# Kernel tuning notes

Measured on AMD Instinct MI355X. Metric: run time of the kernel, lower is better.

The kernel has to match this reference:

```python
import jax, jax.numpy as jnp
import numpy as np
from functools import partial

V, CTX, D, H, L, FF = 50257, 1024, 768, 12, 12, 3072
DH = D // H
EPS = 1e-5


def _ln(x, g, b):
    m = jnp.mean(x, axis=-1, keepdims=True)
    v = jnp.mean(jnp.square(x - m), axis=-1, keepdims=True)
    return (x - m) * jax.lax.rsqrt(v + EPS) * g + b


def setup_inputs() -> dict:
    key = jax.random.key(0)
    ks = jax.random.split(key, 8)
    s = 0.02
    return {
        "input_ids": jax.random.randint(ks[0], (2, 1024), 0, V),
        "token_emb": jax.random.normal(ks[1], (V, D), jnp.float32) * s,
        "pos_emb": jax.random.normal(ks[2], (CTX, D), jnp.float32) * s,
        "ln1_g": jnp.ones((L, D), jnp.float32),
        "ln1_b": jnp.zeros((L, D), jnp.float32),
        "qkv_w": jax.random.normal(ks[3], (L, 3 * D, D), jnp.float32) * s,
        "out_w": jax.random.normal(ks[4], (L, D, D), jnp.float32) * (s / np.sqrt(2 * L)),
        "ln2_g": jnp.ones((L, D), jnp.float32),
        "ln2_b": jnp.zeros((L, D), jnp.float32),
        "ff1_w": jax.random.normal(ks[5], (L, FF, D), jnp.float32) * s,
        "ff2_w": jax.random.normal(ks[6], (L, D, FF), jnp.float32) * s,
        "lnf_g": jnp.ones((D,), jnp.float32),
        "lnf_b": jnp.zeros((D,), jnp.float32),
    }


def reference(input_ids, token_emb, pos_emb, ln1_g, ln1_b, qkv_w, out_w,
              ln2_g, ln2_b, ff1_w, ff2_w, lnf_g, lnf_b):
    B, T = input_ids.shape
    x = token_emb[input_ids] + pos_emb[:T]  # [B,T,D]
    causal = jnp.tril(jnp.ones((T, T), bool))  # True = keep
    scale = 1.0 / np.sqrt(DH)

    def block(x, p):
        g1, b1, wqkv, wo, g2, b2, w1, w2 = p
        h = _ln(x, g1, b1)
        qkv = h @ wqkv.T  # [B,T,3D]
        q, k, v = jnp.split(qkv, 3, axis=-1)
        q = q.reshape(B, T, H, DH).transpose(0, 2, 1, 3)
        k = k.reshape(B, T, H, DH).transpose(0, 2, 1, 3)
        v = v.reshape(B, T, H, DH).transpose(0, 2, 1, 3)
        scores = jnp.einsum('bhqd,bhkd->bhqk', q, k) * scale
        scores = jnp.where(causal, scores, -jnp.inf)
        w = jax.nn.softmax(scores, axis=-1)
        o = jnp.einsum('bhqk,bhkd->bhqd', w, v)
        o = o.transpose(0, 2, 1, 3).reshape(B, T, D) @ wo.T
        x = x + o
        h2 = _ln(x, g2, b2)
        ff = jax.nn.gelu(h2 @ w1.T, approximate=False) @ w2.T
        return x + ff, None

    params = (ln1_g, ln1_b, qkv_w, out_w, ln2_g, ln2_b, ff1_w, ff2_w)
    x, _ = jax.lax.scan(block, x, params)
    x = _ln(x, lnf_g, lnf_b)
    logits = x @ token_emb.T  # tied lm head
    return logits
```

## Files before the change

### kernel.cpp

```cpp
#include <hip/hip_runtime.h>
#include <hip/hip_bf16.h>
#include <math.h>

#define D_MODEL 768
#define NHEAD 12
#define DHEAD 64
#define NLAYER 12
#define FF_DIM 3072
#define SEQ 1024
#define TOKENS 2048
#define VOCAB 50257

typedef short bf16x8 __attribute__((ext_vector_type(8)));
typedef float f32x4 __attribute__((ext_vector_type(4)));
typedef unsigned short u16x4 __attribute__((ext_vector_type(4)));
typedef unsigned short u16x8 __attribute__((ext_vector_type(8)));

__device__ inline unsigned short f2bf(float f) {
    union { float f; unsigned u; } un;
    un.f = f;
    unsigned u = un.u;
    u += 0x7fffu + ((u >> 16) & 1u);
    return (unsigned short)(u >> 16);
}

__device__ inline void gl_lds16(const void* g, void* l) {
    __builtin_amdgcn_global_load_lds(
        (const __attribute__((address_space(1))) unsigned int*)g,
        (__attribute__((address_space(3))) unsigned int*)l, 16, 0, 0);
}

__global__ __launch_bounds__(256) void cvt_kernel(const float* __restrict__ s,
                                                  unsigned short* __restrict__ d,
                                                  long n4) {
    long i = (long)blockIdx.x * 256 + threadIdx.x;
    long stride = (long)gridDim.x * 256;
    for (; i < n4; i += stride) {
        f32x4 v = ((const f32x4*)s)[i];
        u16x4 r;
        r[0] = f2bf(v[0]); r[1] = f2bf(v[1]); r[2] = f2bf(v[2]); r[3] = f2bf(v[3]);
        ((u16x4*)d)[i] = r;
    }
}

__global__ __launch_bounds__(256) void embed_kernel(const int* __restrict__ ids,
                                                    const float* __restrict__ tok,
                                                    const float* __restrict__ pos,
                                                    float* __restrict__ x) {
    int i = blockIdx.x * 256 + threadIdx.x;
    int row = i / D_MODEL;
    int d = i - row * D_MODEL;
    int t = row & (SEQ - 1);
    x[i] = tok[(long)ids[row] * D_MODEL + d] + pos[(long)t * D_MODEL + d];
}

__global__ __launch_bounds__(256) void ln_kernel(const float* __restrict__ x,
                                                 const float* __restrict__ g,
                                                 const float* __restrict__ b,
                                                 unsigned short* __restrict__ out) {
    int row = blockIdx.x;
    int tid = threadIdx.x;
    const float* xr = x + (long)row * D_MODEL;
    float v0 = xr[tid], v1 = xr[tid + 256], v2 = xr[tid + 512];
    __shared__ float sm[4];
    float s = v0 + v1 + v2;
    #pragma unroll
    for (int off = 32; off; off >>= 1) s += __shfl_xor(s, off);
    if ((tid & 63) == 0) sm[tid >> 6] = s;
    __syncthreads();
    float mean = (sm[0] + sm[1] + sm[2] + sm[3]) * (1.f / D_MODEL);
    __syncthreads();
    float d0 = v0 - mean, d1 = v1 - mean, d2 = v2 - mean;
    s = d0 * d0 + d1 * d1 + d2 * d2;
    #pragma unroll
    for (int off = 32; off; off >>= 1) s += __shfl_xor(s, off);
    if ((tid & 63) == 0) sm[tid >> 6] = s;
    __syncthreads();
    float var = (sm[0] + sm[1] + sm[2] + sm[3]) * (1.f / D_MODEL);
    float rs = rsqrtf(var + 1e-5f);
    unsigned short* orow = out + (long)row * D_MODEL;
    orow[tid]       = f2bf(d0 * rs * g[tid]       + b[tid]);
    orow[tid + 256] = f2bf(d1 * rs * g[tid + 256] + b[tid + 256]);
    orow[tid + 512] = f2bf(d2 * rs * g[tid + 512] + b[tid + 512]);
}

#define GM_NONE 0
#define GM_RES  1
#define GM_GELU 2
#define GM_QKV  3

template<int WM, int WN, int MODE, int DB>
__global__ __launch_bounds__(256) void gemm_bf16(
        const unsigned short* __restrict__ A, const unsigned short* __restrict__ W,
        int M, int N, int K,
        float* __restrict__ Cf, unsigned short* __restrict__ Cb,
        const float* __restrict__ RES,
        unsigned short* __restrict__ P1, unsigned short* __restrict__ P2) {
    constexpr int BM = WM * 32, BN = WN * 32;
    __shared__ unsigned short lA[DB][BM * 64];
    __shared__ unsigned short lB[DB][BN * 64];

    int tid = threadIdx.x;
    int lane = tid & 63, wv = tid >> 6;
    int wr = wv >> 1, wc = wv & 1;
    int lr = lane & 15, kq = lane >> 4;
    int row0 = blockIdx.x * BM;
    int col0 = blockIdx.y * BN;

    int srow_in = tid >> 3;
    int ssp = tid & 7;
    int skg = ssp ^ (srow_in & 7);
    int lbase = ((tid & ~63)) << 3;

    f32x4 acc[WM][WN];
    #pragma unroll
    for (int m = 0; m < WM; m++)
        #pragma unroll
        for (int n = 0; n < WN; n++) acc[m][n] = (f32x4){0.f, 0.f, 0.f, 0.f};

    auto stage = [&](int buf, int kt) {
        #pragma unroll
        for (int i = 0; i < BM / 32; i++) {
            int row = i * 32 + srow_in;
            gl_lds16(A + (size_t)(row0 + row) * K + kt + skg * 8,
                     &lA[buf][i * 2048 + lbase]);
        }
        #pragma unroll
        for (int i = 0; i < BN / 32; i++) {
            int row = i * 32 + srow_in;
            int srow = col0 + row;
            if (srow >= N) srow = N - 1;
            gl_lds16(W + (size_t)srow * K + kt + skg * 8,
                     &lB[buf][i * 2048 + lbase]);
        }
    };
    auto compute = [&](int buf) {
        #pragma unroll
        for (int kk = 0; kk < 2; kk++) {
            int kg = kk * 4 + kq;
            bf16x8 af[WM], bfr[WN];
            #pragma unroll
            for (int m = 0; m < WM; m++) {
                int row = wr * (WM * 16) + m * 16 + lr;
                af[m] = *(const bf16x8*)&lA[buf][row * 64 + ((kg ^ (row & 7)) << 3)];
            }
            #pragma unroll
            for (int n = 0; n < WN; n++) {
                int row = wc * (WN * 16) + n * 16 + lr;
                bfr[n] = *(const bf16x8*)&lB[buf][row * 64 + ((kg ^ (row & 7)) << 3)];
            }
            #pragma unroll
            for (int m = 0; m < WM; m++)
                #pragma unroll
                for (int n = 0; n < WN; n++)
                    acc[m][n] = __builtin_amdgcn_mfma_f32_16x16x32_bf16(af[m], bfr[n], acc[m][n], 0, 0, 0);
        }
    };

    if (DB == 2) {
        stage(0, 0);
        __syncthreads();
        int nt = K >> 6;
        int cur = 0;
        for (int t = 0; t < nt; t++) {
            if (t + 1 < nt) stage(cur ^ 1, (t + 1) << 6);
            compute(cur);
            __syncthreads();
            cur ^= 1;
        }
    } else {
        for (int kt = 0; kt < K; kt += 64) {
            stage(0, kt);
            __syncthreads();
            compute(0);
            __syncthreads();
        }
    }

    #pragma unroll
    for (int m = 0; m < WM; m++) {
        int r0 = row0 + wr * (WM * 16) + m * 16 + (kq << 2);
        #pragma unroll
        for (int n = 0; n < WN; n++) {
            int c = col0 + wc * (WN * 16) + n * 16 + lr;
            if (c < N) {
                #pragma unroll
                for (int j = 0; j < 4; j++) {
                    int r = r0 + j;
                    size_t idx = (size_t)r * N + c;
                    float v = acc[m][n][j];
                    if (MODE == GM_RES) {
                        Cf[idx] = v + RES[idx];
                    } else if (MODE == GM_GELU) {
                        Cb[idx] = f2bf(0.5f * v * (1.f + erff(v * 0.70710678118f)));
                    } else if (MODE == GM_QKV) {
                        int bb = r >> 10, t = r & 1023;
                        if (c < D_MODEL) {
                            int h = c >> 6, dh = c & 63;
                            P1[(((size_t)(bb * NHEAD + h) * SEQ) + t) * 64 + dh] = f2bf(v * 0.125f);
                        } else if (c < 2 * D_MODEL) {
                            int cc = c - D_MODEL;
                            int h = cc >> 6, dh = cc & 63;
                            P2[(((size_t)(bb * NHEAD + h) * SEQ) + t) * 64 + dh] = f2bf(v);
                        } else {
                            Cb[(size_t)r * D_MODEL + (c - 2 * D_MODEL)] = f2bf(v);
                        }
                    } else {
                        Cf[idx] = v;
                    }
                }
            }
        }
    }
}

__global__ __launch_bounds__(256) void vprep_kernel(const unsigned short* __restrict__ Vrow,
                                                    unsigned short* __restrict__ Vt) {
    __shared__ unsigned short T[64][66];
    int b = blockIdx.z, h = blockIdx.y, t0 = blockIdx.x * 64;
    int tid = threadIdx.x;
    int tin = tid >> 2, seg = tid & 3;
    const unsigned short* src = Vrow + ((size_t)(b * SEQ) + t0 + tin) * D_MODEL
                                + h * 64 + seg * 16;
    u16x8 a0 = *(const u16x8*)src;
    u16x8 a1 = *(const u16x8*)(src + 8);
    #pragma unroll
    for (int e = 0; e < 8; e++) { T[tin][seg * 16 + e] = a0[e]; T[tin][seg * 16 + 8 + e] = a1[e]; }
    __syncthreads();
    int dh = tid >> 2;
    unsigned short* dst = Vt + ((size_t)(b * NHEAD + h) * 64 + dh) * SEQ + t0 + seg * 16;
    u16x8 o0, o1;
    #pragma unroll
    for (int e = 0; e < 8; e++) o0[e] = T[seg * 16 + e][dh];
    #pragma unroll
    for (int e = 0; e < 8; e++) o1[e] = T[seg * 16 + 8 + e][dh];
    *(u16x8*)dst = o0;
    *(u16x8*)(dst + 8) = o1;
}

#define ANW 4
__global__ __launch_bounds__(256) void attn_mfma(const unsigned short* __restrict__ Qb,
                                                 const unsigned short* __restrict__ Kb,
                                                 const unsigned short* __restrict__ Vt,
                                                 unsigned short* __restrict__ att) {
    int b = blockIdx.z, h = blockIdx.y, pr = blockIdx.x;
    int tid = threadIdx.x, l = tid & 63, w = tid >> 6;
    int lr = l & 15, hg = l >> 4;
    int hk8 = hg * 8, hg4 = hg * 4;
    size_t bh = (size_t)b * NHEAD + h;
    const unsigned short* Qp = Qb + bh * SEQ * 64;
    const unsigned short* Kp = Kb + bh * SEQ * 64;
    const unsigned short* Vp = Vt + bh * 64 * SEQ;

    __shared__ float sm_m[ANW][2][16], sm_l[ANW][2][16];
    __shared__ float sm_o[ANW][2][16][65];
    __shared__ unsigned short pl[ANW][1024];
    unsigned short* Pw = &pl[w][0];

    #pragma unroll
    for (int ti = 0; ti < 2; ti++) {
        int tile = ti ? (63 - pr) : pr;
        int q0 = tile * 16;
        bf16x8 qf0 = *(const bf16x8*)(Qp + (size_t)(q0 + lr) * 64 + hk8);
        bf16x8 qf1 = *(const bf16x8*)(Qp + (size_t)(q0 + lr) * 64 + 32 + hk8);
        f32x4 O[4];
        #pragma unroll
        for (int dt = 0; dt < 4; dt++) O[dt] = (f32x4){0.f, 0.f, 0.f, 0.f};
        f32x4 mrun = (f32x4){-1e30f, -1e30f, -1e30f, -1e30f};
        f32x4 lrun = (f32x4){0.f, 0.f, 0.f, 0.f};
        int nch = (tile >> 2) + 1;

        for (int c = w; c < nch; c += ANW) {
            int k0 = c * 64;
            f32x4 S[4];
            #pragma unroll
            for (int kt = 0; kt < 4; kt++) {
                S[kt] = (f32x4){0.f, 0.f, 0.f, 0.f};
                bf16x8 kf = *(const bf16x8*)(Kp + (size_t)(k0 + kt * 16 + lr) * 64 + hk8);
                S[kt] = __builtin_amdgcn_mfma_f32_16x16x32_bf16(qf0, kf, S[kt], 0, 0, 0);
                kf = *(const bf16x8*)(Kp + (size_t)(k0 + kt * 16 + lr) * 64 + 32 + hk8);
                S[kt] = __builtin_amdgcn_mfma_f32_16x16x32_bf16(qf1, kf, S[kt], 0, 0, 0);
            }
            if (c == nch - 1) {
                #pragma unroll
                for (int kt = 0; kt < 4; kt++)
                    #pragma unroll
                    for (int j = 0; j < 4; j++)
                        S[kt][j] = (k0 + kt * 16 + lr <= q0 + hg4 + j) ? S[kt][j] : -3.0e38f;
            }
            f32x4 rm;
            #pragma unroll
            for (int j = 0; j < 4; j++)
                rm[j] = fmaxf(fmaxf(S[0][j], S[1][j]), fmaxf(S[2][j], S[3][j]));
            #pragma unroll
            for (int msk = 1; msk <= 8; msk <<= 1)
                #pragma unroll
                for (int j = 0; j < 4; j++)
                    rm[j] = fmaxf(rm[j], __shfl_xor(rm[j], msk));
            f32x4 mn, corr, rs;
            #pragma unroll
            for (int j = 0; j < 4; j++) {
                mn[j] = fmaxf(mrun[j], rm[j]);
                corr[j] = __expf(mrun[j] - mn[j]);
                rs[j] = 0.f;
            }
            #pragma unroll
            for (int kt = 0; kt < 4; kt++)
                #pragma unroll
                for (int j = 0; j < 4; j++) {
                    float p = __expf(S[kt][j] - mn[j]);
                    S[kt][j] = p;
                    rs[j] += p;
                }
            #pragma unroll
            for (int msk = 1; msk <= 8; msk <<= 1)
                #pragma unroll
                for (int j = 0; j < 4; j++)
                    rs[j] += __shfl_xor(rs[j], msk);
            #pragma unroll
            for (int j = 0; j < 4; j++) {
                lrun[j] = lrun[j] * corr[j] + rs[j];
                mrun[j] = mn[j];
            }
            #pragma unroll
            for (int dt = 0; dt < 4; dt++)
                #pragma unroll
                for (int j = 0; j < 4; j++) O[dt][j] *= corr[j];
            #pragma unroll
            for (int kt = 0; kt < 4; kt++) {
                int cc = kt * 16 + lr;
                int slot = cc >> 3, off = cc & 7;
                #pragma unroll
                for (int j = 0; j < 4; j++) {
                    int r = hg4 + j;
                    Pw[r * 64 + ((slot ^ (r & 7)) << 3) + off] = f2bf(S[kt][j]);
                }
            }
            asm volatile("s_waitcnt lgkmcnt(0)" ::: "memory");
            bf16x8 pf0 = *(const bf16x8*)&Pw[lr * 64 + ((hg ^ (lr & 7)) << 3)];
            bf16x8 pf1 = *(const bf16x8*)&Pw[lr * 64 + (((4 + hg) ^ (lr & 7)) << 3)];
            #pragma unroll
            for (int dt = 0; dt < 4; dt++) {
                bf16x8 vf = *(const bf16x8*)(Vp + (size_t)(dt * 16 + lr) * SEQ + k0 + hk8);
                O[dt] = __builtin_amdgcn_mfma_f32_16x16x32_bf16(pf0, vf, O[dt], 0, 0, 0);
                vf = *(const bf16x8*)(Vp + (size_t)(dt * 16 + lr) * SEQ + k0 + 32 + hk8);
                O[dt] = __builtin_amdgcn_mfma_f32_16x16x32_bf16(pf1, vf, O[dt], 0, 0, 0);
            }
        }
        if (lr == 0) {
            #pragma unroll
            for (int j = 0; j < 4; j++) {
                sm_m[w][ti][hg4 + j] = mrun[j];
                sm_l[w][ti][hg4 + j] = lrun[j];
            }
        }
        #pragma unroll
        for (int dt = 0; dt < 4; dt++)
            #pragma unroll
            for (int j = 0; j < 4; j++)
                sm_o[w][ti][hg4 + j][dt * 16 + lr] = O[dt][j];
    }
    __syncthreads();
    {
        int ti2 = w >> 1;
        int tile = ti2 ? (63 - pr) : pr;
        int q0 = tile * 16;
        #pragma unroll
        for (int jj = 0; jj < 2; jj++) {
            int j = (w & 1) * 2 + jj;
            int r = hg4 + j;
            float m0 = sm_m[0][ti2][r], m1 = sm_m[1][ti2][r];
            float m2 = sm_m[2][ti2][r], m3 = sm_m[3][ti2][r];
            float M = fmaxf(fmaxf(m0, m1), fmaxf(m2, m3));
            float e0 = __expf(m0 - M), e1 = __expf(m1 - M);
            float e2 = __expf(m2 - M), e3 = __expf(m3 - M);
            float L = sm_l[0][ti2][r] * e0 + sm_l[1][ti2][r] * e1
                    + sm_l[2][ti2][r] * e2 + sm_l[3][ti2][r] * e3;
            float invL = 1.f / L;
            unsigned short* orow = att + ((size_t)(b * SEQ + q0 + r)) * D_MODEL + h * 64;
            #pragma unroll
            for (int dt = 0; dt < 4; dt++) {
                int cidx = dt * 16 + lr;
                float o = sm_o[0][ti2][r][cidx] * e0 + sm_o[1][ti2][r][cidx] * e1
                        + sm_o[2][ti2][r][cidx] * e2 + sm_o[3][ti2][r][cidx] * e3;
                orow[cidx] = f2bf(o * invL);
            }
        }
    }
}

extern "C" void kernel_launch(void* const* d_in, const int* in_sizes, int n_in,
                              void* d_out, int out_size, void* d_ws, size_t ws_size,
                              hipStream_t stream) {
    const int*   input_ids = (const int*)d_in[0];
    const float* token_emb = (const float*)d_in[1];
    const float* pos_emb   = (const float*)d_in[2];
    const float* ln1_g     = (const float*)d_in[3];
    const float* ln1_b     = (const float*)d_in[4];
    const float* qkv_w     = (const float*)d_in[5];
    const float* out_w     = (const float*)d_in[6];
    const float* ln2_g     = (const float*)d_in[7];
    const float* ln2_b     = (const float*)d_in[8];
    const float* ff1_w     = (const float*)d_in[9];
    const float* ff2_w     = (const float*)d_in[10];
    const float* lnf_g     = (const float*)d_in[11];
    const float* lnf_b     = (const float*)d_in[12];
    float* out = (float*)d_out;

    const size_t SZ_QKV_L = (size_t)3 * D_MODEL * D_MODEL;
    const size_t SZ_OUT_L = (size_t)D_MODEL * D_MODEL;
    const size_t SZ_FF1_L = (size_t)FF_DIM * D_MODEL;
    const size_t SZ_FF2_L = (size_t)D_MODEL * FF_DIM;
    const size_t SZ_TOK   = (size_t)VOCAB * D_MODEL;

    char* base = (char*)d_ws;
    size_t off = 0;
    auto alloc = [&](size_t bytes) -> char* {
        char* p = base + off;
        off = (off + bytes + 255) & ~(size_t)255;
        return p;
    };

    float* x              = (float*)alloc((size_t)TOKENS * D_MODEL * 4);
    unsigned short* hb    = (unsigned short*)alloc((size_t)TOKENS * D_MODEL * 2);
    unsigned short* attb  = (unsigned short*)alloc((size_t)TOKENS * D_MODEL * 2);
    unsigned short* ffab  = (unsigned short*)alloc((size_t)TOKENS * FF_DIM * 2);
    unsigned short* Qb    = (unsigned short*)alloc((size_t)TOKENS * D_MODEL * 2);
    unsigned short* Kb    = (unsigned short*)alloc((size_t)TOKENS * D_MODEL * 2);
    unsigned short* Vrow  = (unsigned short*)alloc((size_t)TOKENS * D_MODEL * 2);
    unsigned short* Vtb   = (unsigned short*)alloc((size_t)TOKENS * D_MODEL * 2);

    size_t act_end = off;
    size_t full_need = act_end + 2 * (NLAYER * (SZ_QKV_L + SZ_OUT_L + SZ_FF1_L + SZ_FF2_L) + SZ_TOK)
                       + 6 * 256;
    bool full = ws_size >= full_need;

    unsigned short *qkvA, *outA, *ff1A, *ff2A, *tokA;
    if (full) {
        qkvA = (unsigned short*)alloc(2 * NLAYER * SZ_QKV_L);
        outA = (unsigned short*)alloc(2 * NLAYER * SZ_OUT_L);
        ff1A = (unsigned short*)alloc(2 * NLAYER * SZ_FF1_L);
        ff2A = (unsigned short*)alloc(2 * NLAYER * SZ_FF2_L);
        tokA = (unsigned short*)alloc(2 * SZ_TOK);
    } else {
        qkvA = (unsigned short*)alloc(2 * SZ_QKV_L);
        outA = (unsigned short*)alloc(2 * SZ_OUT_L);
        ff1A = (unsigned short*)alloc(2 * SZ_FF1_L);
        ff2A = (unsigned short*)alloc(2 * SZ_FF2_L);
        tokA = (unsigned short*)alloc(2 * SZ_TOK);
    }

    auto cvt = [&](const float* s, unsigned short* d, size_t n) {
        long n4 = (long)(n / 4);
        int g = (int)((n4 + 255) / 256);
        if (g > 2048) g = 2048;
        cvt_kernel<<<g, 256, 0, stream>>>(s, d, n4);
    };

    if (full) {
        cvt(qkv_w, qkvA, NLAYER * SZ_QKV_L);
        cvt(out_w, outA, NLAYER * SZ_OUT_L);
        cvt(ff1_w, ff1A, NLAYER * SZ_FF1_L);
        cvt(ff2_w, ff2A, NLAYER * SZ_FF2_L);
        cvt(token_emb, tokA, SZ_TOK);
    }

    embed_kernel<<<TOKENS * D_MODEL / 256, 256, 0, stream>>>(input_ids, token_emb, pos_emb, x);

    for (int l = 0; l < NLAYER; l++) {
        const unsigned short* qw = full ? qkvA + (size_t)l * SZ_QKV_L : qkvA;
        const unsigned short* ow = full ? outA + (size_t)l * SZ_OUT_L : outA;
        const unsigned short* f1 = full ? ff1A + (size_t)l * SZ_FF1_L : ff1A;
        const unsigned short* f2 = full ? ff2A + (size_t)l * SZ_FF2_L : ff2A;

        ln_kernel<<<TOKENS, 256, 0, stream>>>(x, ln1_g + l * D_MODEL, ln1_b + l * D_MODEL, hb);
        if (!full) cvt(qkv_w + (size_t)l * SZ_QKV_L, qkvA, SZ_QKV_L);
        gemm_bf16<2, 4, GM_QKV, 2><<<dim3(TOKENS / 64, 3 * D_MODEL / 128), 256, 0, stream>>>(
            hb, qw, TOKENS, 3 * D_MODEL, D_MODEL, nullptr, Vrow, nullptr, Qb, Kb);
        vprep_kernel<<<dim3(SEQ / 64, NHEAD, 2), 256, 0, stream>>>(Vrow, Vtb);
        attn_mfma<<<dim3(32, NHEAD, 2), 256, 0, stream>>>(Qb, Kb, Vtb, attb);
        if (!full) cvt(out_w + (size_t)l * SZ_OUT_L, outA, SZ_OUT_L);
        gemm_bf16<2, 2, GM_RES, 2><<<dim3(TOKENS / 64, D_MODEL / 64), 256, 0, stream>>>(
            attb, ow, TOKENS, D_MODEL, D_MODEL, x, nullptr, x, nullptr, nullptr);
        ln_kernel<<<TOKENS, 256, 0, stream>>>(x, ln2_g + l * D_MODEL, ln2_b + l * D_MODEL, hb);
        if (!full) cvt(ff1_w + (size_t)l * SZ_FF1_L, ff1A, SZ_FF1_L);
        gemm_bf16<2, 4, GM_GELU, 2><<<dim3(TOKENS / 64, FF_DIM / 128), 256, 0, stream>>>(
            hb, f1, TOKENS, FF_DIM, D_MODEL, nullptr, ffab, nullptr, nullptr, nullptr);
        if (!full) cvt(ff2_w + (size_t)l * SZ_FF2_L, ff2A, SZ_FF2_L);
        gemm_bf16<2, 2, GM_RES, 2><<<dim3(TOKENS / 64, D_MODEL / 64), 256, 0, stream>>>(
            ffab, f2, TOKENS, D_MODEL, FF_DIM, x, nullptr, x, nullptr, nullptr);
    }

    ln_kernel<<<TOKENS, 256, 0, stream>>>(x, lnf_g, lnf_b, hb);
    if (!full) cvt(token_emb, tokA, SZ_TOK);
    gemm_bf16<4, 4, GM_NONE, 2><<<dim3(TOKENS / 128, (VOCAB + 127) / 128), 256, 0, stream>>>(
        hb, tokA, TOKENS, VOCAB, D_MODEL, out, nullptr, nullptr, nullptr, nullptr);
}
```

Before: 2.198 ms.

## Fuse V transpose into QKV GEMM epilogue and retune GEMM tile shapes

The QKV GEMM epilogue now writes V directly in transposed head-major layout as 4-element vector stores, so the separate vprep transpose kernel and its intermediate buffer are removed. Q/K stores compute the base address once per fragment. Tile shapes are also changed: QKV and FF1 use WN=3 (96-wide column tiles) and the residual GEMMs use WM=1 (32-row tiles), which gives more blocks on a GPU with many CUs. The risks are a less coalesced strided transposed store and lower per-block reuse with the smaller tiles.

```diff
diff --git a/kernel.cpp b/kernel.cpp
--- a/kernel.cpp
+++ b/kernel.cpp
@@ -184,58 +184,47 @@
         for (int n = 0; n < WN; n++) {
             int c = col0 + wc * (WN * 16) + n * 16 + lr;
             if (c < N) {
-                #pragma unroll
-                for (int j = 0; j < 4; j++) {
-                    int r = r0 + j;
-                    size_t idx = (size_t)r * N + c;
-                    float v = acc[m][n][j];
-                    if (MODE == GM_RES) {
-                        Cf[idx] = v + RES[idx];
-                    } else if (MODE == GM_GELU) {
-                        Cb[idx] = f2bf(0.5f * v * (1.f + erff(v * 0.70710678118f)));
-                    } else if (MODE == GM_QKV) {
-                        int bb = r >> 10, t = r & 1023;
-                        if (c < D_MODEL) {
-                            int h = c >> 6, dh = c & 63;
-                            P1[(((size_t)(bb * NHEAD + h) * SEQ) + t) * 64 + dh] = f2bf(v * 0.125f);
-                        } else if (c < 2 * D_MODEL) {
-                            int cc = c - D_MODEL;
-                            int h = cc >> 6, dh = cc & 63;
-                            P2[(((size_t)(bb * NHEAD + h) * SEQ) + t) * 64 + dh] = f2bf(v);
+                if (MODE == GM_QKV) {
+                    int bb = r0 >> 10, t0q = r0 & 1023;
+                    if (c < D_MODEL) {
+                        int h = c >> 6, dh = c & 63;
+                        size_t base = (((size_t)(bb * NHEAD + h) * SEQ) + t0q) * 64 + dh;
+                        #pragma unroll
+                        for (int j = 0; j < 4; j++)
+                            P1[base + (size_t)j * 64] = f2bf(acc[m][n][j] * 0.125f);
+                    } else if (c < 2 * D_MODEL) {
+                        int cc = c - D_MODEL;
+                        int h = cc >> 6, dh = cc & 63;
+                        size_t base = (((size_t)(bb * NHEAD + h) * SEQ) + t0q) * 64 + dh;
+                        #pragma unroll
+                        for (int j = 0; j < 4; j++)
+                            P2[base + (size_t)j * 64] = f2bf(acc[m][n][j]);
+                    } else {
+                        int cc = c - 2 * D_MODEL;
+                        int h = cc >> 6, dh = cc & 63;
+                        u16x4 vv;
+                        #pragma unroll
+                        for (int j = 0; j < 4; j++) vv[j] = f2bf(acc[m][n][j]);
+                        *(u16x4*)(Cb + ((size_t)(bb * NHEAD + h) * 64 + dh) * SEQ + t0q) = vv;
+                    }
+                } else {
+                    #pragma unroll
+                    for (int j = 0; j < 4; j++) {
+                        int r = r0 + j;
+                        size_t idx = (size_t)r * N + c;
+                        float v = acc[m][n][j];
+                        if (MODE == GM_RES) {
+                            Cf[idx] = v + RES[idx];
+                        } else if (MODE == GM_GELU) {
+                            Cb[idx] = f2bf(0.5f * v * (1.f + erff(v * 0.70710678118f)));
                         } else {
-                            Cb[(size_t)r * D_MODEL + (c - 2 * D_MODEL)] = f2bf(v);
+                            Cf[idx] = v;
                         }
-                    } else {
-                        Cf[idx] = v;
                     }
                 }
             }
         }
     }
-}
-
-__global__ __launch_bounds__(256) void vprep_kernel(const unsigned short* __restrict__ Vrow,
-                                                    unsigned short* __restrict__ Vt) {
-    __shared__ unsigned short T[64][66];
-    int b = blockIdx.z, h = blockIdx.y, t0 = blockIdx.x * 64;
-    int tid = threadIdx.x;
-    int tin = tid >> 2, seg = tid & 3;
-    const unsigned short* src = Vrow + ((size_t)(b * SEQ) + t0 + tin) * D_MODEL
-                                + h * 64 + seg * 16;
-    u16x8 a0 = *(const u16x8*)src;
-    u16x8 a1 = *(const u16x8*)(src + 8);
-    #pragma unroll
-    for (int e = 0; e < 8; e++) { T[tin][seg * 16 + e] = a0[e]; T[tin][seg * 16 + 8 + e] = a1[e]; }
-    __syncthreads();
-    int dh = tid >> 2;
-    unsigned short* dst = Vt + ((size_t)(b * NHEAD + h) * 64 + dh) * SEQ + t0 + seg * 16;
-    u16x8 o0, o1;
-    #pragma unroll
-    for (int e = 0; e < 8; e++) o0[e] = T[seg * 16 + e][dh];
-    #pragma unroll
-    for (int e = 0; e < 8; e++) o1[e] = T[seg * 16 + 8 + e][dh];
-    *(u16x8*)dst = o0;
-    *(u16x8*)(dst + 8) = o1;
 }
 
 #define ANW 4
@@ -427,7 +416,6 @@
     unsigned short* ffab  = (unsigned short*)alloc((size_t)TOKENS * FF_DIM * 2);
     unsigned short* Qb    = (unsigned short*)alloc((size_t)TOKENS * D_MODEL * 2);
     unsigned short* Kb    = (unsigned short*)alloc((size_t)TOKENS * D_MODEL * 2);
-    unsigned short* Vrow  = (unsigned short*)alloc((size_t)TOKENS * D_MODEL * 2);
     unsigned short* Vtb   = (unsigned short*)alloc((size_t)TOKENS * D_MODEL * 2);
 
     size_t act_end = off;
@@ -475,19 +463,18 @@
 
         ln_kernel<<<TOKENS, 256, 0, stream>>>(x, ln1_g + l * D_MODEL, ln1_b + l * D_MODEL, hb);
         if (!full) cvt(qkv_w + (size_t)l * SZ_QKV_L, qkvA, SZ_QKV_L);
-        gemm_bf16<2, 4, GM_QKV, 2><<<dim3(TOKENS / 64, 3 * D_MODEL / 128), 256, 0, stream>>>(
-            hb, qw, TOKENS, 3 * D_MODEL, D_MODEL, nullptr, Vrow, nullptr, Qb, Kb);
-        vprep_kernel<<<dim3(SEQ / 64, NHEAD, 2), 256, 0, stream>>>(Vrow, Vtb);
+        gemm_bf16<2, 3, GM_QKV, 2><<<dim3(TOKENS / 64, 3 * D_MODEL / 96), 256, 0, stream>>>(
+            hb, qw, TOKENS, 3 * D_MODEL, D_MODEL, nullptr, Vtb, nullptr, Qb, Kb);
         attn_mfma<<<dim3(32, NHEAD, 2), 256, 0, stream>>>(Qb, Kb, Vtb, attb);
         if (!full) cvt(out_w + (size_t)l * SZ_OUT_L, outA, SZ_OUT_L);
-        gemm_bf16<2, 2, GM_RES, 2><<<dim3(TOKENS / 64, D_MODEL / 64), 256, 0, stream>>>(
+        gemm_bf16<1, 2, GM_RES, 2><<<dim3(TOKENS / 32, D_MODEL / 64), 256, 0, stream>>>(
             attb, ow, TOKENS, D_MODEL, D_MODEL, x, nullptr, x, nullptr, nullptr);
         ln_kernel<<<TOKENS, 256, 0, stream>>>(x, ln2_g + l * D_MODEL, ln2_b + l * D_MODEL, hb);
         if (!full) cvt(ff1_w + (size_t)l * SZ_FF1_L, ff1A, SZ_FF1_L);
-        gemm_bf16<2, 4, GM_GELU, 2><<<dim3(TOKENS / 64, FF_DIM / 128), 256, 0, stream>>>(
+        gemm_bf16<2, 3, GM_GELU, 2><<<dim3(TOKENS / 64, FF_DIM / 96), 256, 0, stream>>>(
             hb, f1, TOKENS, FF_DIM, D_MODEL, nullptr, ffab, nullptr, nullptr, nullptr);
         if (!full) cvt(ff2_w + (size_t)l * SZ_FF2_L, ff2A, SZ_FF2_L);
-        gemm_bf16<2, 2, GM_RES, 2><<<dim3(TOKENS / 64, D_MODEL / 64), 256, 0, stream>>>(
+        gemm_bf16<1, 2, GM_RES, 2><<<dim3(TOKENS / 32, D_MODEL / 64), 256, 0, stream>>>(
             ffab, f2, TOKENS, D_MODEL, FF_DIM, x, nullptr, x, nullptr, nullptr);
     }
 
```

Result: faster. 2.036 ms (-7.3%).
